# Optimization experiments

Measured on AMD Instinct MI355X. Metric: run time of the kernel, lower is better.

The kernel has to match this reference:

```python
import jax, jax.numpy as jnp
import numpy as np

D_MODEL = 1024
NUM_HEADS = 16
HEAD_DIM = D_MODEL // NUM_HEADS
B, L = 4, 4096


def _linear(x, w, b):
    # torch nn.Linear: y = x @ w.T + b, w: [out, in]
    return jnp.einsum('bld,od->blo', x, w) + b


def _elu_feature_map(x):
    return jax.nn.elu(x) + 1.0


def setup_inputs() -> dict:
    key = jax.random.key(0)
    ks = jax.random.split(key, 11)
    s = 1.0 / np.sqrt(D_MODEL)
    inp = {
        'query': jax.random.normal(ks[0], (B, L, D_MODEL), jnp.float32),
        'key': jax.random.normal(ks[1], (B, L, D_MODEL), jnp.float32),
        'value': jax.random.normal(ks[2], (B, L, D_MODEL), jnp.float32),
        'wq': jax.random.uniform(ks[3], (D_MODEL, D_MODEL), jnp.float32, -s, s),
        'bq': jax.random.uniform(ks[4], (D_MODEL,), jnp.float32, -s, s),
        'wk': jax.random.uniform(ks[5], (D_MODEL, D_MODEL), jnp.float32, -s, s),
        'bk': jax.random.uniform(ks[6], (D_MODEL,), jnp.float32, -s, s),
        'wv': jax.random.uniform(ks[7], (D_MODEL, D_MODEL), jnp.float32, -s, s),
        'bv': jax.random.uniform(ks[8], (D_MODEL,), jnp.float32, -s, s),
        'wo': jax.random.uniform(ks[9], (D_MODEL, D_MODEL), jnp.float32, -s, s),
        'bo': jax.random.uniform(ks[10], (D_MODEL,), jnp.float32, -s, s),
    }
    return inp


def reference(query, key, value, wq, bq, wk, bk, wv, bv, wo, bo):
    Bsz, Lq, _ = query.shape
    # project and split heads -> [B, H, L, hd]
    def split_heads(x):
        return x.reshape(Bsz, -1, NUM_HEADS, HEAD_DIM).transpose(0, 2, 1, 3)
    Q = split_heads(_linear(query, wq, bq))
    K = split_heads(_linear(key, wk, bk))
    V = split_heads(_linear(value, wv, bv))
    Q = _elu_feature_map(Q)
    K = _elu_feature_map(K)
    # KV: [B, H, hd, hd]
    KV = jnp.einsum('bhld,bhle->bhde', K, V)
    Ksum = K.sum(axis=2)  # [B, H, hd]
    Z = 1.0 / (jnp.einsum('bhld,bhd->bhl', Q, Ksum) + 1e-6)  # [B, H, Lq]
    out = jnp.einsum('bhld,bhde->bhle', Q, KV) * Z[..., None]
    out = out.transpose(0, 2, 1, 3).reshape(Bsz, Lq, D_MODEL)
    return _linear(out, wo, bo)
```

## Files before the change

kernel.cpp:

```cpp
#include <hip/hip_runtime.h>
#include <hip/hip_bf16.h>

typedef _Float16 half8 __attribute__((ext_vector_type(8)));
typedef _Float16 half4 __attribute__((ext_vector_type(4)));
typedef float f32x4 __attribute__((ext_vector_type(4)));

#define KDIM 1024
#define NDIM 1024
#define MROWS 16384

#define GLD_LDS16(g, l)                                                  \
  __builtin_amdgcn_global_load_lds(                                      \
      (const __attribute__((address_space(1))) void*)(g),                \
      (__attribute__((address_space(3))) void*)(l), 16, 0, 0)

__global__ __launch_bounds__(256)
void cvt_f32_to_f16(const float* __restrict__ src, _Float16* __restrict__ dst,
                    int n8) {
  for (int i = blockIdx.x * 256 + threadIdx.x; i < n8; i += gridDim.x * 256) {
    float4 f0 = ((const float4*)src)[2 * i];
    float4 f1 = ((const float4*)src)[2 * i + 1];
    half8 h;
    h[0] = (_Float16)f0.x; h[1] = (_Float16)f0.y;
    h[2] = (_Float16)f0.z; h[3] = (_Float16)f0.w;
    h[4] = (_Float16)f1.x; h[5] = (_Float16)f1.y;
    h[6] = (_Float16)f1.z; h[7] = (_Float16)f1.w;
    ((half8*)dst)[i] = h;
  }
}

template <int ACT, int TRANS, typename TOUT>
__global__ __launch_bounds__(256, 2)
void gemm_h(const _Float16* __restrict__ X, const _Float16* __restrict__ W,
            const float* __restrict__ bias, TOUT* __restrict__ Y) {
  constexpr int BM = 128, BN = 128, BK = 64;
  __shared__ _Float16 As[BM * BK];
  __shared__ _Float16 Bs[BN * BK];
  const int tid  = threadIdx.x;
  const int lane = tid & 63;
  const int w    = tid >> 6;
  const int wr   = (w >> 1) * 64;
  const int wc   = (w & 1) * 64;
  const int m0   = blockIdx.x * BM;
  const int n0   = blockIdx.y * BN;

  const int lr = lane >> 3;
  const int ls = (lane & 7) ^ lr;
  const _Float16* gA = X + (size_t)(m0 + w * 32 + lr) * KDIM + ls * 8;
  const _Float16* gB = W + (size_t)(n0 + w * 32 + lr) * KDIM + ls * 8;
  _Float16* ldsA = As + (w * 32) * BK;
  _Float16* ldsB = Bs + (w * 32) * BK;

  f32x4 acc[4][4] = {};

  for (int k0 = 0; k0 < KDIM; k0 += BK) {
    __syncthreads();
#pragma unroll
    for (int c = 0; c < 4; ++c) {
      GLD_LDS16(gA + k0 + (size_t)(c * 8) * KDIM, ldsA + c * 8 * BK);
      GLD_LDS16(gB + k0 + (size_t)(c * 8) * KDIM, ldsB + c * 8 * BK);
    }
    __syncthreads();

    half8 afr[4][2], bfr[4][2];
#pragma unroll
    for (int m = 0; m < 4; ++m)
#pragma unroll
      for (int kk = 0; kk < 2; ++kk) {
        int row  = wr + m * 16 + (lane & 15);
        int byte = row * 128 + ((lane >> 4) << 4) + kk * 64;
        byte ^= (row & 7) << 4;
        afr[m][kk] = *(const half8*)((const char*)As + byte);
      }
#pragma unroll
    for (int n = 0; n < 4; ++n)
#pragma unroll
      for (int kk = 0; kk < 2; ++kk) {
        int row  = wc + n * 16 + (lane & 15);
        int byte = row * 128 + ((lane >> 4) << 4) + kk * 64;
        byte ^= (row & 7) << 4;
        bfr[n][kk] = *(const half8*)((const char*)Bs + byte);
      }
#pragma unroll
    for (int kk = 0; kk < 2; ++kk)
#pragma unroll
      for (int m = 0; m < 4; ++m)
#pragma unroll
        for (int n = 0; n < 4; ++n)
          acc[m][n] = __builtin_amdgcn_mfma_f32_16x16x32_f16(afr[m][kk], bfr[n][kk],
                                                             acc[m][n], 0, 0, 0);
  }

#pragma unroll
  for (int n = 0; n < 4; ++n) {
    int col  = n0 + wc + n * 16 + (lane & 15);
    float bv = bias[col];
#pragma unroll
    for (int m = 0; m < 4; ++m) {
      int r0 = m0 + wr + m * 16 + ((lane >> 4) << 2);
      if constexpr (TRANS) {
        int b  = r0 >> 12;
        int l0 = r0 & 4095;
        half4 hv;
#pragma unroll
        for (int i = 0; i < 4; ++i) {
          float v = acc[m][n][i] + bv;
          if constexpr (ACT == 1) v = (v > 0.f) ? (v + 1.f) : __expf(v);
          hv[i] = (_Float16)v;
        }
        *(half4*)((_Float16*)Y + ((size_t)(b * 1024 + col)) * 4096 + l0) = hv;
      } else {
#pragma unroll
        for (int i = 0; i < 4; ++i) {
          float v = acc[m][n][i] + bv;
          if constexpr (ACT == 1) v = (v > 0.f) ? (v + 1.f) : __expf(v);
          Y[(size_t)(r0 + i) * NDIM + col] = (TOUT)v;
        }
      }
    }
  }
}

__global__ __launch_bounds__(256, 2)
void kv_mfma(const _Float16* __restrict__ KT, const _Float16* __restrict__ VT,
             _Float16* __restrict__ pKV) {
  const int bh = blockIdx.x;
  const int ch = blockIdx.y;
  const int tid  = threadIdx.x;
  const int lane = tid & 63;
  const int w    = tid >> 6;

  __shared__ _Float16 As[64 * 64];
  __shared__ _Float16 Bs[64 * 64];

  const int lr = lane >> 3;
  const int ls = (lane & 7) ^ lr;
  const size_t lbase = (size_t)ch * 512 + ls * 8;
  const _Float16* gA = VT + (size_t)(bh * 64 + w * 16 + lr) * 4096 + lbase;
  const _Float16* gB = KT + (size_t)(bh * 64 + w * 16 + lr) * 4096 + lbase;
  _Float16* ldsA = As + (w * 16) * 64;
  _Float16* ldsB = Bs + (w * 16) * 64;

  half8 aones;
#pragma unroll
  for (int j = 0; j < 8; ++j) aones[j] = (lane & 15) == 0 ? (_Float16)1.0f : (_Float16)0.0f;

  f32x4 acc[5] = {};

  for (int k0 = 0; k0 < 512; k0 += 64) {
    __syncthreads();
#pragma unroll
    for (int c = 0; c < 2; ++c) {
      GLD_LDS16(gA + k0 + (size_t)(c * 8) * 4096, ldsA + c * 8 * 64);
      GLD_LDS16(gB + k0 + (size_t)(c * 8) * 4096, ldsB + c * 8 * 64);
    }
    __syncthreads();

    half8 afr[4][2], bfr[2];
#pragma unroll
    for (int m = 0; m < 4; ++m)
#pragma unroll
      for (int kk = 0; kk < 2; ++kk) {
        int row  = m * 16 + (lane & 15);
        int byte = row * 128 + ((lane >> 4) << 4) + kk * 64;
        byte ^= (row & 7) << 4;
        afr[m][kk] = *(const half8*)((const char*)As + byte);
      }
#pragma unroll
    for (int kk = 0; kk < 2; ++kk) {
      int row  = w * 16 + (lane & 15);
      int byte = row * 128 + ((lane >> 4) << 4) + kk * 64;
      byte ^= (row & 7) << 4;
      bfr[kk] = *(const half8*)((const char*)Bs + byte);
    }
#pragma unroll
    for (int kk = 0; kk < 2; ++kk) {
#pragma unroll
      for (int m = 0; m < 4; ++m)
        acc[m] = __builtin_amdgcn_mfma_f32_16x16x32_f16(afr[m][kk], bfr[kk],
                                                        acc[m], 0, 0, 0);
      acc[4] = __builtin_amdgcn_mfma_f32_16x16x32_f16(aones, bfr[kk],
                                                      acc[4], 0, 0, 0);
    }
  }

  _Float16* outp = pKV + ((size_t)ch * 64 + bh) * 5120;
  const int col = w * 16 + (lane & 15);
#pragma unroll
  for (int m = 0; m < 5; ++m) {
#pragma unroll
    for (int i = 0; i < 4; ++i) {
      int row = m * 16 + ((lane >> 4) << 2) + i;
      outp[row * 64 + col] = (_Float16)acc[m][i];
    }
  }
}

__global__ __launch_bounds__(256)
void kv_combine(const _Float16* __restrict__ pKV, _Float16* __restrict__ KVTx) {
  int g = blockIdx.x * 256 + threadIdx.x;
  int bh = g / 5120;
  int j  = g - bh * 5120;
  float s = 0.f;
#pragma unroll
  for (int ch = 0; ch < 8; ++ch)
    s += (float)pKV[((size_t)ch * 64 + bh) * 5120 + j];
  KVTx[(size_t)bh * 5120 + j] = (_Float16)s;
}

__global__ __launch_bounds__(256, 2)
void attn_kernel(const _Float16* __restrict__ Qp, const _Float16* __restrict__ KVTx,
                 _Float16* __restrict__ att) {
  const int mt = blockIdx.x;
  const int bh = blockIdx.y;
  const int b  = bh >> 4, h = bh & 15;
  const int tid = threadIdx.x;
  const int lane = tid & 63;
  const int w = tid >> 6;
  const size_t m0 = (size_t)b * 4096 + (size_t)mt * 128;

  __shared__ _Float16 As[128 * 64];
  __shared__ _Float16 Bs[80 * 64];

#pragma unroll
  for (int j = 0; j < 4; ++j) {
    int c    = tid + 256 * j;
    int row  = c >> 3;
    int col8 = (c & 7) << 3;
    int byte = row * 128 + (col8 << 1);
    byte ^= (row & 7) << 4;
    *(half8*)((char*)As + byte) =
        *(const half8*)(Qp + (m0 + row) * KDIM + h * 64 + col8);
  }
  for (int c = tid; c < 640; c += 256) {
    int row  = c >> 3;
    int col8 = (c & 7) << 3;
    int byte = row * 128 + (col8 << 1);
    byte ^= (row & 7) << 4;
    *(half8*)((char*)Bs + byte) = *(const half8*)(KVTx + (size_t)bh * 5120 + c * 8);
  }
  __syncthreads();

  f32x4 acc[2][5] = {};
  half8 afr[2][2], bfr[5][2];
#pragma unroll
  for (int m = 0; m < 2; ++m)
#pragma unroll
    for (int kk = 0; kk < 2; ++kk) {
      int row  = w * 32 + m * 16 + (lane & 15);
      int byte = row * 128 + ((lane >> 4) << 4) + kk * 64;
      byte ^= (row & 7) << 4;
      afr[m][kk] = *(const half8*)((const char*)As + byte);
    }
#pragma unroll
  for (int n = 0; n < 5; ++n)
#pragma unroll
    for (int kk = 0; kk < 2; ++kk) {
      int row  = n * 16 + (lane & 15);
      int byte = row * 128 + ((lane >> 4) << 4) + kk * 64;
      byte ^= (row & 7) << 4;
      bfr[n][kk] = *(const half8*)((const char*)Bs + byte);
    }
#pragma unroll
  for (int kk = 0; kk < 2; ++kk)
#pragma unroll
    for (int m = 0; m < 2; ++m)
#pragma unroll
      for (int n = 0; n < 5; ++n)
        acc[m][n] = __builtin_amdgcn_mfma_f32_16x16x32_f16(afr[m][kk], bfr[n][kk],
                                                           acc[m][n], 0, 0, 0);

#pragma unroll
  for (int m = 0; m < 2; ++m) {
#pragma unroll
    for (int i = 0; i < 4; ++i) {
      float dn = __shfl(acc[m][4][i], lane & 48);
      float z  = 1.f / (dn + 1e-6f);
      size_t row = m0 + w * 32 + m * 16 + ((lane >> 4) << 2) + i;
#pragma unroll
      for (int n = 0; n < 4; ++n) {
        att[row * NDIM + h * 64 + n * 16 + (lane & 15)] =
            (_Float16)(acc[m][n][i] * z);
      }
    }
  }
}

extern "C" void kernel_launch(void* const* d_in, const int* in_sizes, int n_in,
                              void* d_out, int out_size, void* d_ws, size_t ws_size,
                              hipStream_t stream) {
  const float* q  = (const float*)d_in[0];
  const float* k  = (const float*)d_in[1];
  const float* v  = (const float*)d_in[2];
  const float* wq = (const float*)d_in[3];
  const float* bq = (const float*)d_in[4];
  const float* wk = (const float*)d_in[5];
  const float* bk = (const float*)d_in[6];
  const float* wv = (const float*)d_in[7];
  const float* bv = (const float*)d_in[8];
  const float* wo = (const float*)d_in[9];
  const float* bo = (const float*)d_in[10];
  float* out = (float*)d_out;

  char* ws = (char*)d_ws;
  _Float16* Qp   = (_Float16*)(ws);
  _Float16* KT   = (_Float16*)(ws + 33554432);
  _Float16* VT   = (_Float16*)(ws + 67108864);
  _Float16* Wh   = (_Float16*)(ws + 100663296);
  _Float16* pKVh = (_Float16*)(ws + 102760448);
  _Float16* KVTx = (_Float16*)(ws + 108003328);
  _Float16* att  = KT;
  _Float16* Xh   = (_Float16*)d_out;

  const int N8_BIG = MROWS * KDIM / 8;
  const int N8_W   = KDIM * KDIM / 8;

  dim3 gproj(MROWS / 128, NDIM / 128);

  cvt_f32_to_f16<<<2048, 256, 0, stream>>>(q, Xh, N8_BIG);
  cvt_f32_to_f16<<<512, 256, 0, stream>>>(wq, Wh, N8_W);
  gemm_h<1, 0, _Float16><<<gproj, 256, 0, stream>>>(Xh, Wh, bq, Qp);
  cvt_f32_to_f16<<<2048, 256, 0, stream>>>(k, Xh, N8_BIG);
  cvt_f32_to_f16<<<512, 256, 0, stream>>>(wk, Wh, N8_W);
  gemm_h<1, 1, _Float16><<<gproj, 256, 0, stream>>>(Xh, Wh, bk, KT);
  cvt_f32_to_f16<<<2048, 256, 0, stream>>>(v, Xh, N8_BIG);
  cvt_f32_to_f16<<<512, 256, 0, stream>>>(wv, Wh, N8_W);
  gemm_h<0, 1, _Float16><<<gproj, 256, 0, stream>>>(Xh, Wh, bv, VT);

  kv_mfma<<<dim3(64, 8), 256, 0, stream>>>(KT, VT, pKVh);
  kv_combine<<<1280, 256, 0, stream>>>(pKVh, KVTx);

  attn_kernel<<<dim3(32, 64), 256, 0, stream>>>(Qp, KVTx, att);

  cvt_f32_to_f16<<<512, 256, 0, stream>>>(wo, Wh, N8_W);
  gemm_h<0, 0, float><<<gproj, 256, 0, stream>>>(att, Wh, bo, out);
}
```

Before: 280.7 us.

## Replace projection GEMM with 256x128 tile, triple-buffered LDS pipeline

The four projection GEMMs move to a new kernel with 512 threads and 256x128 tiles. It uses a three-stage LDS ring buffer, so global-to-LDS loads for tile t+2 overlap the MFMAs on tile t, and the two barriers per k-step become one wait-and-barrier. The kernel also remaps block IDs into a grouped order for better L2 reuse and raises wave priority around the MFMA block. In exchange, LDS use rises to about 144KB per block, which can cap occupancy at one block per CU despite the launch bound of two.

```diff
diff --git a/kernel.cpp b/kernel.cpp
--- a/kernel.cpp
+++ b/kernel.cpp
@@ -30,81 +30,110 @@
 }
 
 template <int ACT, int TRANS, typename TOUT>
-__global__ __launch_bounds__(256, 2)
-void gemm_h(const _Float16* __restrict__ X, const _Float16* __restrict__ W,
-            const float* __restrict__ bias, TOUT* __restrict__ Y) {
-  constexpr int BM = 128, BN = 128, BK = 64;
-  __shared__ _Float16 As[BM * BK];
-  __shared__ _Float16 Bs[BN * BK];
+__global__ __launch_bounds__(512, 2)
+void gemm_big(const _Float16* __restrict__ X, const _Float16* __restrict__ W,
+              const float* __restrict__ bias, TOUT* __restrict__ Y) {
+  constexpr int BM = 256, BN = 128, BK = 64;
+  __shared__ _Float16 As[3 * BM * BK];
+  __shared__ _Float16 Bs[3 * BN * BK];
+
   const int tid  = threadIdx.x;
   const int lane = tid & 63;
   const int w    = tid >> 6;
-  const int wr   = (w >> 1) * 64;
-  const int wc   = (w & 1) * 64;
-  const int m0   = blockIdx.x * BM;
-  const int n0   = blockIdx.y * BN;
+  const int wm   = w >> 1;
+  const int wn   = w & 1;
+
+  const int bid = blockIdx.x;
+  const int wid = (bid & 7) * 64 + (bid >> 3);
+  const int m0  = (wid >> 3) * BM;
+  const int n0  = (wid & 7) * BN;
 
   const int lr = lane >> 3;
   const int ls = (lane & 7) ^ lr;
-  const _Float16* gA = X + (size_t)(m0 + w * 32 + lr) * KDIM + ls * 8;
-  const _Float16* gB = W + (size_t)(n0 + w * 32 + lr) * KDIM + ls * 8;
-  _Float16* ldsA = As + (w * 32) * BK;
-  _Float16* ldsB = Bs + (w * 32) * BK;
+
+#define STAGE_TILE(kt, bidx)                                                  \
+  {                                                                           \
+    const int k0s = (kt) * BK;                                                \
+    _Float16* la = As + (bidx) * (BM * BK) + w * 512;                         \
+    _Float16* lb = Bs + (bidx) * (BN * BK) + w * 512;                         \
+    _Pragma("unroll")                                                         \
+    for (int j = 0; j < 4; ++j)                                               \
+      GLD_LDS16(X + (size_t)(m0 + w * 8 + 64 * j + lr) * KDIM + k0s + ls * 8, \
+                la + 4096 * j);                                               \
+    _Pragma("unroll")                                                         \
+    for (int j = 0; j < 2; ++j)                                               \
+      GLD_LDS16(W + (size_t)(n0 + w * 8 + 64 * j + lr) * KDIM + k0s + ls * 8, \
+                lb + 4096 * j);                                               \
+  }
 
   f32x4 acc[4][4] = {};
 
-  for (int k0 = 0; k0 < KDIM; k0 += BK) {
-    __syncthreads();
-#pragma unroll
-    for (int c = 0; c < 4; ++c) {
-      GLD_LDS16(gA + k0 + (size_t)(c * 8) * KDIM, ldsA + c * 8 * BK);
-      GLD_LDS16(gB + k0 + (size_t)(c * 8) * KDIM, ldsB + c * 8 * BK);
-    }
-    __syncthreads();
+  STAGE_TILE(0, 0);
+  STAGE_TILE(1, 1);
+  asm volatile("s_waitcnt vmcnt(6)" ::: "memory");
+  asm volatile("s_barrier" ::: "memory");
+
+  int bc = 0;
+  for (int t = 0; t < 16; ++t) {
+    int bs = bc + 2; if (bs >= 3) bs -= 3;
+    const char* Ab = (const char*)As + bc * (BM * BK * 2);
+    const char* Bb = (const char*)Bs + bc * (BN * BK * 2);
 
     half8 afr[4][2], bfr[4][2];
 #pragma unroll
-    for (int m = 0; m < 4; ++m)
+    for (int mi = 0; mi < 4; ++mi)
 #pragma unroll
       for (int kk = 0; kk < 2; ++kk) {
-        int row  = wr + m * 16 + (lane & 15);
+        int row  = wm * 64 + mi * 16 + (lane & 15);
         int byte = row * 128 + ((lane >> 4) << 4) + kk * 64;
         byte ^= (row & 7) << 4;
-        afr[m][kk] = *(const half8*)((const char*)As + byte);
-      }
-#pragma unroll
-    for (int n = 0; n < 4; ++n)
+        afr[mi][kk] = *(const half8*)(Ab + byte);
+      }
+#pragma unroll
+    for (int ni = 0; ni < 4; ++ni)
 #pragma unroll
       for (int kk = 0; kk < 2; ++kk) {
-        int row  = wc + n * 16 + (lane & 15);
+        int row  = wn * 64 + ni * 16 + (lane & 15);
         int byte = row * 128 + ((lane >> 4) << 4) + kk * 64;
         byte ^= (row & 7) << 4;
-        bfr[n][kk] = *(const half8*)((const char*)Bs + byte);
-      }
+        bfr[ni][kk] = *(const half8*)(Bb + byte);
+      }
+
+    if (t < 14) STAGE_TILE(t + 2, bs);
+
+    __builtin_amdgcn_s_setprio(1);
 #pragma unroll
     for (int kk = 0; kk < 2; ++kk)
 #pragma unroll
-      for (int m = 0; m < 4; ++m)
-#pragma unroll
-        for (int n = 0; n < 4; ++n)
-          acc[m][n] = __builtin_amdgcn_mfma_f32_16x16x32_f16(afr[m][kk], bfr[n][kk],
-                                                             acc[m][n], 0, 0, 0);
-  }
-
-#pragma unroll
-  for (int n = 0; n < 4; ++n) {
-    int col  = n0 + wc + n * 16 + (lane & 15);
+      for (int mi = 0; mi < 4; ++mi)
+#pragma unroll
+        for (int ni = 0; ni < 4; ++ni)
+          acc[mi][ni] = __builtin_amdgcn_mfma_f32_16x16x32_f16(
+              afr[mi][kk], bfr[ni][kk], acc[mi][ni], 0, 0, 0);
+    __builtin_amdgcn_s_setprio(0);
+
+    if (t < 15) {
+      asm volatile("s_waitcnt vmcnt(6)" ::: "memory");
+      asm volatile("s_barrier" ::: "memory");
+    }
+    ++bc; if (bc == 3) bc = 0;
+  }
+#undef STAGE_TILE
+
+#pragma unroll
+  for (int ni = 0; ni < 4; ++ni) {
+    int col  = n0 + wn * 64 + ni * 16 + (lane & 15);
     float bv = bias[col];
 #pragma unroll
-    for (int m = 0; m < 4; ++m) {
-      int r0 = m0 + wr + m * 16 + ((lane >> 4) << 2);
+    for (int mi = 0; mi < 4; ++mi) {
+      int r0 = m0 + wm * 64 + mi * 16 + ((lane >> 4) << 2);
       if constexpr (TRANS) {
         int b  = r0 >> 12;
         int l0 = r0 & 4095;
         half4 hv;
 #pragma unroll
         for (int i = 0; i < 4; ++i) {
-          float v = acc[m][n][i] + bv;
+          float v = acc[mi][ni][i] + bv;
           if constexpr (ACT == 1) v = (v > 0.f) ? (v + 1.f) : __expf(v);
           hv[i] = (_Float16)v;
         }
@@ -112,7 +141,7 @@
       } else {
 #pragma unroll
         for (int i = 0; i < 4; ++i) {
-          float v = acc[m][n][i] + bv;
+          float v = acc[mi][ni][i] + bv;
           if constexpr (ACT == 1) v = (v > 0.f) ? (v + 1.f) : __expf(v);
           Y[(size_t)(r0 + i) * NDIM + col] = (TOUT)v;
         }
@@ -315,17 +344,17 @@
   const int N8_BIG = MROWS * KDIM / 8;
   const int N8_W   = KDIM * KDIM / 8;
 
-  dim3 gproj(MROWS / 128, NDIM / 128);
+  const int GBLK = (MROWS / 256) * (NDIM / 128);
 
   cvt_f32_to_f16<<<2048, 256, 0, stream>>>(q, Xh, N8_BIG);
   cvt_f32_to_f16<<<512, 256, 0, stream>>>(wq, Wh, N8_W);
-  gemm_h<1, 0, _Float16><<<gproj, 256, 0, stream>>>(Xh, Wh, bq, Qp);
+  gemm_big<1, 0, _Float16><<<GBLK, 512, 0, stream>>>(Xh, Wh, bq, Qp);
   cvt_f32_to_f16<<<2048, 256, 0, stream>>>(k, Xh, N8_BIG);
   cvt_f32_to_f16<<<512, 256, 0, stream>>>(wk, Wh, N8_W);
-  gemm_h<1, 1, _Float16><<<gproj, 256, 0, stream>>>(Xh, Wh, bk, KT);
+  gemm_big<1, 1, _Float16><<<GBLK, 512, 0, stream>>>(Xh, Wh, bk, KT);
   cvt_f32_to_f16<<<2048, 256, 0, stream>>>(v, Xh, N8_BIG);
   cvt_f32_to_f16<<<512, 256, 0, stream>>>(wv, Wh, N8_W);
-  gemm_h<0, 1, _Float16><<<gproj, 256, 0, stream>>>(Xh, Wh, bv, VT);
+  gemm_big<0, 1, _Float16><<<GBLK, 512, 0, stream>>>(Xh, Wh, bv, VT);
 
   kv_mfma<<<dim3(64, 8), 256, 0, stream>>>(KT, VT, pKVh);
   kv_combine<<<1280, 256, 0, stream>>>(pKVh, KVTx);
@@ -333,5 +362,5 @@
   attn_kernel<<<dim3(32, 64), 256, 0, stream>>>(Qp, KVTx, att);
 
   cvt_f32_to_f16<<<512, 256, 0, stream>>>(wo, Wh, N8_W);
-  gemm_h<0, 0, float><<<gproj, 256, 0, stream>>>(att, Wh, bo, out);
-}
+  gemm_big<0, 0, float><<<GBLK, 512, 0, stream>>>(att, Wh, bo, out);
+}
```

Measured after the change: 273.4 us. 2.6% less time.

## Replace projection GEMM with 256x256 tile, 8-wave double-buffered pipelined kernel

Applied to the files above, without the earlier changes.

Swaps the 128x128 single-buffered projection GEMM for a 256x256 tile kernel with 8 waves, double-buffered LDS and four phases per K-step. Each phase prefetches the next K-half with global_load_lds while MFMAs run, and uses raw s_barrier with explicit vmcnt waits and setprio. Block IDs are remapped for L2 locality. The goal is to hide global-load latency, remove the two full syncthreads per K-step and raise arithmetic intensity. In exchange it uses 128KB LDS and more accumulator registers per block, and the hand-counted waitcnt values are fragile.

```diff
diff --git a/kernel.cpp b/kernel.cpp
--- a/kernel.cpp
+++ b/kernel.cpp
@@ -13,6 +13,8 @@
   __builtin_amdgcn_global_load_lds(                                      \
       (const __attribute__((address_space(1))) void*)(g),                \
       (__attribute__((address_space(3))) void*)(l), 16, 0, 0)
+
+#define SBAR asm volatile("s_barrier" ::: "memory")
 
 __global__ __launch_bounds__(256)
 void cvt_f32_to_f16(const float* __restrict__ src, _Float16* __restrict__ dst,
@@ -30,81 +32,108 @@
 }
 
 template <int ACT, int TRANS, typename TOUT>
-__global__ __launch_bounds__(256, 2)
-void gemm_h(const _Float16* __restrict__ X, const _Float16* __restrict__ W,
-            const float* __restrict__ bias, TOUT* __restrict__ Y) {
-  constexpr int BM = 128, BN = 128, BK = 64;
-  __shared__ _Float16 As[BM * BK];
-  __shared__ _Float16 Bs[BN * BK];
+__global__ __launch_bounds__(512, 2)
+void gemm_8p(const _Float16* __restrict__ X, const _Float16* __restrict__ W,
+             const float* __restrict__ bias, TOUT* __restrict__ Y) {
+  __shared__ _Float16 As[2 * 2 * 8192];
+  __shared__ _Float16 Bs[2 * 2 * 8192];
+
   const int tid  = threadIdx.x;
   const int lane = tid & 63;
   const int w    = tid >> 6;
-  const int wr   = (w >> 1) * 64;
-  const int wc   = (w & 1) * 64;
-  const int m0   = blockIdx.x * BM;
-  const int n0   = blockIdx.y * BN;
-
-  const int lr = lane >> 3;
-  const int ls = (lane & 7) ^ lr;
-  const _Float16* gA = X + (size_t)(m0 + w * 32 + lr) * KDIM + ls * 8;
-  const _Float16* gB = W + (size_t)(n0 + w * 32 + lr) * KDIM + ls * 8;
-  _Float16* ldsA = As + (w * 32) * BK;
-  _Float16* ldsB = Bs + (w * 32) * BK;
-
-  f32x4 acc[4][4] = {};
-
-  for (int k0 = 0; k0 < KDIM; k0 += BK) {
-    __syncthreads();
-#pragma unroll
-    for (int c = 0; c < 4; ++c) {
-      GLD_LDS16(gA + k0 + (size_t)(c * 8) * KDIM, ldsA + c * 8 * BK);
-      GLD_LDS16(gB + k0 + (size_t)(c * 8) * KDIM, ldsB + c * 8 * BK);
-    }
-    __syncthreads();
-
-    half8 afr[4][2], bfr[4][2];
-#pragma unroll
-    for (int m = 0; m < 4; ++m)
-#pragma unroll
-      for (int kk = 0; kk < 2; ++kk) {
-        int row  = wr + m * 16 + (lane & 15);
-        int byte = row * 128 + ((lane >> 4) << 4) + kk * 64;
-        byte ^= (row & 7) << 4;
-        afr[m][kk] = *(const half8*)((const char*)As + byte);
-      }
-#pragma unroll
-    for (int n = 0; n < 4; ++n)
-#pragma unroll
-      for (int kk = 0; kk < 2; ++kk) {
-        int row  = wc + n * 16 + (lane & 15);
-        int byte = row * 128 + ((lane >> 4) << 4) + kk * 64;
-        byte ^= (row & 7) << 4;
-        bfr[n][kk] = *(const half8*)((const char*)Bs + byte);
-      }
-#pragma unroll
-    for (int kk = 0; kk < 2; ++kk)
-#pragma unroll
-      for (int m = 0; m < 4; ++m)
-#pragma unroll
-        for (int n = 0; n < 4; ++n)
-          acc[m][n] = __builtin_amdgcn_mfma_f32_16x16x32_f16(afr[m][kk], bfr[n][kk],
-                                                             acc[m][n], 0, 0, 0);
-  }
-
-#pragma unroll
-  for (int n = 0; n < 4; ++n) {
-    int col  = n0 + wc + n * 16 + (lane & 15);
+  const int wm   = w >> 2;
+  const int wn   = w & 3;
+
+  const int bid = blockIdx.x;
+  const int wid = (bid & 7) * 32 + (bid >> 3);
+  const int m0  = (wid >> 2) * 256;
+  const int n0  = (wid & 3) * 256;
+
+  const int srow = w * 16 + (lane >> 2);
+  const int ssl  = (lane & 3) ^ ((lane >> 3) & 3);
+  const _Float16* gA = X + (size_t)(m0 + srow) * KDIM + ssl * 8;
+  const _Float16* gB = W + (size_t)(n0 + srow) * KDIM + ssl * 8;
+  _Float16* lA = As + (size_t)(w * 64 + lane) * 8;
+  _Float16* lB = Bs + (size_t)(w * 64 + lane) * 8;
+  const int rsl = ((lane >> 4) ^ ((lane >> 1) & 3)) << 4;
+
+  f32x4 acc[8][4] = {};
+
+#define STAGE(GP, LP, Tt, KH)                                              \
+  {                                                                        \
+    _Pragma("unroll")                                                      \
+    for (int j = 0; j < 2; ++j)                                            \
+      GLD_LDS16(GP + (size_t)j * 128 * KDIM + (Tt) * 64 + (KH) * 32,       \
+                LP + ((Tt) & 1) * 16384 + (KH) * 8192 + j * 4096);         \
+  }
+
+#define PHASE(MH, KH, STG, WEND)                                           \
+  {                                                                        \
+    const char* Ab = (const char*)As + d * 32768 + (KH) * 16384;           \
+    const char* Bb = (const char*)Bs + d * 32768 + (KH) * 16384;           \
+    half8 afr[4], bfr[4];                                                  \
+    _Pragma("unroll")                                                      \
+    for (int mi = 0; mi < 4; ++mi) {                                       \
+      int r = wm * 128 + (MH) * 64 + mi * 16 + (lane & 15);                \
+      afr[mi] = *(const half8*)(Ab + r * 64 + rsl);                        \
+    }                                                                      \
+    _Pragma("unroll")                                                      \
+    for (int ni = 0; ni < 4; ++ni) {                                       \
+      int r = wn * 64 + ni * 16 + (lane & 15);                             \
+      bfr[ni] = *(const half8*)(Bb + r * 64 + rsl);                        \
+    }                                                                      \
+    STG;                                                                   \
+    SBAR;                                                                  \
+    __builtin_amdgcn_s_setprio(1);                                         \
+    _Pragma("unroll")                                                      \
+    for (int mi = 0; mi < 4; ++mi)                                         \
+      _Pragma("unroll")                                                    \
+      for (int ni = 0; ni < 4; ++ni)                                       \
+        acc[(MH) * 4 + mi][ni] = __builtin_amdgcn_mfma_f32_16x16x32_f16(   \
+            afr[mi], bfr[ni], acc[(MH) * 4 + mi][ni], 0, 0, 0);            \
+    __builtin_amdgcn_s_setprio(0);                                         \
+    WEND;                                                                  \
+    SBAR;                                                                  \
+  }
+
+  STAGE(gA, lA, 0, 0); STAGE(gB, lB, 0, 0);
+  STAGE(gA, lA, 0, 1); STAGE(gB, lB, 0, 1);
+  STAGE(gA, lA, 1, 0); STAGE(gB, lB, 1, 0);
+  asm volatile("s_waitcnt vmcnt(4)" ::: "memory");
+  SBAR;
+
+  for (int T = 0; T < 16; ++T) {
+    const int d = T & 1;
+    PHASE(0, 0, { if (T < 15) STAGE(gA, lA, T + 1, 1); }, {});
+    PHASE(1, 0, { if (T < 15) STAGE(gB, lB, T + 1, 1); },
+          {
+            if (T < 15) { asm volatile("s_waitcnt vmcnt(8)" ::: "memory"); }
+            else        { asm volatile("s_waitcnt vmcnt(0)" ::: "memory"); }
+          });
+    PHASE(0, 1, { if (T < 14) STAGE(gA, lA, T + 2, 0); }, {});
+    PHASE(1, 1, { if (T < 14) STAGE(gB, lB, T + 2, 0); },
+          {
+            if (T < 14)       { asm volatile("s_waitcnt vmcnt(8)" ::: "memory"); }
+            else if (T == 14) { asm volatile("s_waitcnt vmcnt(4)" ::: "memory"); }
+          });
+  }
+#undef STAGE
+#undef PHASE
+
+#pragma unroll
+  for (int ni = 0; ni < 4; ++ni) {
+    int col  = n0 + wn * 64 + ni * 16 + (lane & 15);
     float bv = bias[col];
 #pragma unroll
-    for (int m = 0; m < 4; ++m) {
-      int r0 = m0 + wr + m * 16 + ((lane >> 4) << 2);
+    for (int mi = 0; mi < 8; ++mi) {
+      int r0 = m0 + wm * 128 + mi * 16 + ((lane >> 4) << 2);
       if constexpr (TRANS) {
         int b  = r0 >> 12;
         int l0 = r0 & 4095;
         half4 hv;
 #pragma unroll
         for (int i = 0; i < 4; ++i) {
-          float v = acc[m][n][i] + bv;
+          float v = acc[mi][ni][i] + bv;
           if constexpr (ACT == 1) v = (v > 0.f) ? (v + 1.f) : __expf(v);
           hv[i] = (_Float16)v;
         }
@@ -112,7 +141,7 @@
       } else {
 #pragma unroll
         for (int i = 0; i < 4; ++i) {
-          float v = acc[m][n][i] + bv;
+          float v = acc[mi][ni][i] + bv;
           if constexpr (ACT == 1) v = (v > 0.f) ? (v + 1.f) : __expf(v);
           Y[(size_t)(r0 + i) * NDIM + col] = (TOUT)v;
         }
@@ -315,17 +344,17 @@
   const int N8_BIG = MROWS * KDIM / 8;
   const int N8_W   = KDIM * KDIM / 8;
 
-  dim3 gproj(MROWS / 128, NDIM / 128);
+  const int GBLK = (MROWS / 256) * (NDIM / 256);
 
   cvt_f32_to_f16<<<2048, 256, 0, stream>>>(q, Xh, N8_BIG);
   cvt_f32_to_f16<<<512, 256, 0, stream>>>(wq, Wh, N8_W);
-  gemm_h<1, 0, _Float16><<<gproj, 256, 0, stream>>>(Xh, Wh, bq, Qp);
+  gemm_8p<1, 0, _Float16><<<GBLK, 512, 0, stream>>>(Xh, Wh, bq, Qp);
   cvt_f32_to_f16<<<2048, 256, 0, stream>>>(k, Xh, N8_BIG);
   cvt_f32_to_f16<<<512, 256, 0, stream>>>(wk, Wh, N8_W);
-  gemm_h<1, 1, _Float16><<<gproj, 256, 0, stream>>>(Xh, Wh, bk, KT);
+  gemm_8p<1, 1, _Float16><<<GBLK, 512, 0, stream>>>(Xh, Wh, bk, KT);
   cvt_f32_to_f16<<<2048, 256, 0, stream>>>(v, Xh, N8_BIG);
   cvt_f32_to_f16<<<512, 256, 0, stream>>>(wv, Wh, N8_W);
-  gemm_h<0, 1, _Float16><<<gproj, 256, 0, stream>>>(Xh, Wh, bv, VT);
+  gemm_8p<0, 1, _Float16><<<GBLK, 512, 0, stream>>>(Xh, Wh, bv, VT);
 
   kv_mfma<<<dim3(64, 8), 256, 0, stream>>>(KT, VT, pKVh);
   kv_combine<<<1280, 256, 0, stream>>>(pKVh, KVTx);
@@ -333,5 +362,5 @@
   attn_kernel<<<dim3(32, 64), 256, 0, stream>>>(Qp, KVTx, att);
 
   cvt_f32_to_f16<<<512, 256, 0, stream>>>(wo, Wh, N8_W);
-  gemm_h<0, 0, float><<<gproj, 256, 0, stream>>>(att, Wh, bo, out);
-}
+  gemm_8p<0, 0, float><<<GBLK, 512, 0, stream>>>(att, Wh, bo, out);
+}
```

New measurement: 272.8 us. 1.03x faster.
